# Kernel tuning notes

Hardware: AMD Instinct MI355X
Metric: run time of the kernel (lower is better)

Reference implementation:

```python
import jax, jax.numpy as jnp
import numpy as np

NUM_PERSISTENT = 16
ALIBI_ALPHA = 1.0
START_I = 0
DILATION = 1
LN_EPS = 1e-5


def setup_inputs() -> dict:
    key = jax.random.key(0)
    ks = jax.random.split(key, 16)
    B, S, C, H = 8, 1024, 512, 8
    D = C // H
    P = NUM_PERSISTENT
    Kk = 3
    x = jax.random.normal(ks[0], (B, S, C), dtype=jnp.float32)
    mask = jnp.ones((B, 1, S, S), dtype=jnp.int32)
    sc = 0.02
    Wq = jax.random.normal(ks[1], (D, D), jnp.float32) * sc
    Wk = jax.random.normal(ks[2], (D, D), jnp.float32) * sc
    Wv = jax.random.normal(ks[3], (D, D), jnp.float32) * sc
    pk = jax.random.normal(ks[4], (P, H, D), jnp.float32) * sc
    pv = jax.random.normal(ks[5], (P, H, D), jnp.float32) * sc
    th_pre = jax.random.normal(ks[6], (H, H), jnp.float32) * (1.0 / np.sqrt(H))
    th_post = jax.random.normal(ks[7], (H, H), jnp.float32) * (1.0 / np.sqrt(H))
    fc_w = jax.random.normal(ks[8], (C, C), jnp.float32) * sc
    fc_b = jnp.zeros((C,), jnp.float32)
    conv1_w = jax.random.normal(ks[9], (C, C, Kk), jnp.float32) * 0.01
    conv1_b = jnp.zeros((C,), jnp.float32)
    conv2_w = jax.random.normal(ks[10], (C, C, Kk), jnp.float32) * 0.01
    conv2_b = jnp.zeros((C,), jnp.float32)
    ln_g = jnp.ones((C,), jnp.float32)
    ln_b = jnp.zeros((C,), jnp.float32)
    return dict(x=x, mask=mask, Wq=Wq, Wk=Wk, Wv=Wv, pk=pk, pv=pv,
                th_pre=th_pre, th_post=th_post, fc_w=fc_w, fc_b=fc_b,
                conv1_w=conv1_w, conv1_b=conv1_b, conv2_w=conv2_w,
                conv2_b=conv2_b, ln_g=ln_g, ln_b=ln_b)


def _causal_conv(x_nct, w_oik, b_o, dilation):
    # padding (k-1)*d on both sides + chomp right == pad left only
    k = w_oik.shape[-1]
    p = (k - 1) * dilation
    y = jax.lax.conv_general_dilated(
        x_nct, w_oik, window_strides=(1,), padding=[(p, 0)],
        rhs_dilation=(dilation,), dimension_numbers=("NCH", "OIH", "NCH"))
    return y + b_o[None, :, None]


def reference(x, mask, Wq, Wk, Wv, pk, pv, th_pre, th_post, fc_w, fc_b,
              conv1_w, conv1_b, conv2_w, conv2_b, ln_g, ln_b):
    N, S, C = x.shape
    H = th_pre.shape[0]
    D = C // H
    P = pk.shape[0]

    # ---- MultiHeadAttention (eval: dropout = identity) ----
    xh = x.reshape(N, S, H, D)
    q = jnp.einsum("nshd,ed->nshe", xh, Wq)
    k = jnp.einsum("nshd,ed->nshe", xh, Wk)
    v = jnp.einsum("nshd,ed->nshe", xh, Wv)
    # persistent memory tokens appended along key/value length
    k = jnp.concatenate([k, jnp.broadcast_to(pk[None], (N, P, H, D))], axis=1)
    v = jnp.concatenate([v, jnp.broadcast_to(pv[None], (N, P, H, D))], axis=1)

    energy = jnp.einsum("nqhd,nkhd->nhqk", q, k)  # (N,H,S,S+P)

    # ALiBi bias (symmetric |q-k|), zero over persistent keys
    slopes = 2.0 ** (-(ALIBI_ALPHA * (jnp.arange(1, H + 1, dtype=jnp.float32) + START_I)))
    t = jnp.arange(S, dtype=jnp.float32)
    dist = jnp.abs(t[:, None] - t[None, :])  # (S,S)
    bias = -dist[None, None] * slopes[None, :, None, None]  # (1,H,S,S)
    bias = jnp.pad(bias, ((0, 0), (0, 0), (0, 0), (0, P)))
    energy = energy + bias

    # pre-softmax talking heads (1x1 conv over head axis)
    energy = jnp.einsum("hg,ngqk->nhqk", th_pre, energy)

    ext_mask = jnp.pad(mask, ((0, 0), (0, 0), (0, 0), (0, P)), constant_values=1)
    energy = jnp.where(ext_mask == 0, jnp.float32(-1e4), energy)

    attn = jax.nn.softmax(energy / jnp.sqrt(jnp.float32(C)), axis=-1)
    attn = jnp.einsum("hg,ngqk->nhqk", th_post, attn)

    att_out = jnp.einsum("nhql,nlhd->nqhd", attn, v).reshape(N, S, C)
    att_out = att_out @ fc_w.T + fc_b

    x = x + att_out  # residual (dropout1 identity in eval)

    # ---- TemporalBlock (causal dilated convs, no SE since heads>0) ----
    xc = jnp.transpose(x, (0, 2, 1))  # (N,C,S)
    h = jax.nn.relu(_causal_conv(xc, conv1_w, conv1_b, DILATION))
    h = jax.nn.relu(_causal_conv(h, conv2_w, conv2_b, DILATION))
    out = jax.nn.relu(h + xc)  # downsample is None (in==out)

    # mask out invalid frames
    conv_mask = mask[:, 0, :, 0][:, None, :]  # (N,1,S)
    out = jnp.where(conv_mask == 0, 0.0, out)

    y = jnp.transpose(out, (0, 2, 1))  # (N,S,C)
    mu = jnp.mean(y, axis=-1, keepdims=True)
    var = jnp.mean(jnp.square(y - mu), axis=-1, keepdims=True)
    y = (y - mu) * jax.lax.rsqrt(var + LN_EPS) * ln_g + ln_b
    return y
```

## Files before the change

kernel.cpp:

```cpp
#include <hip/hip_runtime.h>
#include <hip/hip_bf16.h>

#define BN 8
#define SS 1024
#define CC 512
#define HH 8
#define DD 64
#define PP 16
#define KT 1040
#define KTE 1088

typedef __hip_bfloat16 bf16;
typedef unsigned char uchar;
typedef unsigned short ushort;
typedef unsigned int uint;
typedef __attribute__((ext_vector_type(8))) short short8;
typedef __attribute__((ext_vector_type(4))) float f32x4;
typedef __attribute__((ext_vector_type(2))) float f32x2;

__device__ __forceinline__ short f2s(float v){ bf16 b = __float2bfloat16(v); return *(short*)&b; }
__device__ __forceinline__ float s2f(short s){ bf16 b; *(short*)&b = s; return __bfloat162float(b); }
__device__ __forceinline__ uchar f2q(float v){
    return (uchar)__builtin_amdgcn_cvt_pk_fp8_f32(v, v, 0, false);
}
__device__ __forceinline__ float rfl(float x){
    return __int_as_float(__builtin_amdgcn_readfirstlane(__float_as_int(x)));
}

#define MFMA16(a,b,c)  __builtin_amdgcn_mfma_f32_16x16x32_bf16(a,b,c,0,0,0)
#define MFMAF8(a,b,c)  __builtin_amdgcn_mfma_f32_16x16x32_fp8_fp8(a,b,c,0,0,0)

__global__ __launch_bounds__(256) void prep_kernel(
    const float* __restrict__ fc_w, const float* __restrict__ c1w,
    const float* __restrict__ c2w, const float* __restrict__ Wq,
    const float* __restrict__ Wk, const float* __restrict__ Wv,
    const float* __restrict__ th_post,
    const float* __restrict__ pk, const float* __restrict__ pv,
    short* __restrict__ Bfc, uchar* __restrict__ Bc1,
    uchar* __restrict__ Bc2, short* __restrict__ Bqkv,
    uchar* __restrict__ kf, uchar* __restrict__ vt)
{
    int i = blockIdx.x*256 + threadIdx.x;
    const int NFC = 512*512, NCV = 512*1536, NQ = 3*64*64, NP = BN*HH*PP*DD;
    if (i < NFC) {
        int c = i >> 9, r = i & 511;
        int g = r >> 6, d = r & 63;
        float s = 0.f;
        #pragma unroll
        for (int h = 0; h < 8; ++h)
            s += fc_w[(size_t)c*512 + h*64 + d] * th_post[h*8 + g];
        Bfc[i] = f2s(s);
        return;
    }
    i -= NFC;
    if (i < NCV) {
        int o = i/1536, r = i%1536, dk = r>>9, ci = r&511;
        Bc1[i] = f2q(c1w[(o*512+ci)*3+dk] * 16.f); return;
    }
    i -= NCV;
    if (i < NCV) {
        int o = i/1536, r = i%1536, dk = r>>9, ci = r&511;
        Bc2[i] = f2q(c2w[(o*512+ci)*3+dk] * 16.f); return;
    }
    i -= NCV;
    if (i < NQ) {
        int w = i >> 12, rest = i & 4095;
        const float* W = (w==0)?Wq:(w==1)?Wk:Wv;
        Bqkv[i] = f2s(W[((rest>>6)&63)*64 + (rest&63)]);
        return;
    }
    i -= NQ;
    if (i < NP) {
        int d = i & 63, p = (i >> 6) & 15, h = (i >> 10) & 7, n = i >> 13;
        size_t src = ((size_t)p*HH + h)*DD + d;
        kf[(((size_t)(n*HH+h))*KT + SS + p)*DD + d] = f2q(pk[src]);
        vt[(((size_t)(n*HH+h))*DD + d)*KT + SS + p] = f2q(pv[src]);
    }
}

__global__ __launch_bounds__(256) void qkv_mfma(
    const float* __restrict__ x, const short* __restrict__ Bqkv,
    uchar* __restrict__ qf, uchar* __restrict__ kf, uchar* __restrict__ vt)
{
    __shared__ short Xs[64*72];
    __shared__ short Ws[192*72];
    const int tid = threadIdx.x;
    const int lin = blockIdx.x;
    const int xcd = lin & 7, slot = lin >> 3;
    const int m0 = (xcd*16 + (slot & 15))*64;
    const int h = slot >> 4;
    const int wave = tid >> 6, lane = tid & 63;
    const int lr = lane & 15, lq = lane >> 4;

    for (int i = tid; i < 1024; i += 256) {
        int r = i >> 4, cg = (i & 15)*4;
        float4 v = *(const float4*)(x + (size_t)(m0+r)*CC + h*64 + cg);
        Xs[r*72+cg+0] = f2s(v.x); Xs[r*72+cg+1] = f2s(v.y);
        Xs[r*72+cg+2] = f2s(v.z); Xs[r*72+cg+3] = f2s(v.w);
    }
    for (int i = tid; i < 3072; i += 256) {
        int r = i >> 4, cg = (i & 15)*4;
        *(short4*)(Ws + r*72 + cg) = *(const short4*)(Bqkv + (size_t)r*64 + cg);
    }
    __syncthreads();

    f32x4 acc[12];
    #pragma unroll
    for (int nt = 0; nt < 12; ++nt) acc[nt] = {0.f,0.f,0.f,0.f};
    #pragma unroll
    for (int ks = 0; ks < 2; ++ks) {
        int ko = ks*32 + lq*8;
        short8 a = *(const short8*)(Xs + (wave*16 + lr)*72 + ko);
        #pragma unroll
        for (int nt = 0; nt < 12; ++nt) {
            short8 b = *(const short8*)(Ws + (nt*16 + lr)*72 + ko);
            acc[nt] = MFMA16(a, b, acc[nt]);
        }
    }
    #pragma unroll
    for (int nt = 0; nt < 12; ++nt) {
        int ep = nt*16 + lr;
        int w = ep >> 6, e = ep & 63;
        #pragma unroll
        for (int reg = 0; reg < 4; ++reg) {
            int m = m0 + wave*16 + lq*4 + reg;
            int n = m >> 10, s = m & 1023;
            float v = acc[nt][reg];
            if (w == 0)      qf[((size_t)(n*HH+h)*SS + s)*DD + e] = f2q(v);
            else if (w == 1) kf[((size_t)(n*HH+h)*KT + s)*DD + e] = f2q(v);
            else             vt[(((size_t)(n*HH+h))*DD + e)*KT + s] = f2q(v);
        }
    }
}

__device__ __forceinline__ void en_loadK(const uchar* __restrict__ kf,
    int nh, int kt, int tid, uint2* rk)
{
    #pragma unroll
    for (int j = 0; j < 2; ++j) {
        int i = tid + j*256;
        int r = i >> 3, c8 = (i & 7)*8;
        int kcol = kt*64 + r;
        uint2 v = {0u, 0u};
        if (kcol < KT)
            v = *(const uint2*)(kf + ((size_t)nh*KT + kcol)*DD + c8);
        rk[j] = v;
    }
}

__global__ __launch_bounds__(256) void energy_mfma8(
    const uchar* __restrict__ qf, const uchar* __restrict__ kf,
    uchar* __restrict__ E)
{
    __shared__ uchar Qs[64*72];
    __shared__ uchar Ks[64*72];
    const int tid = threadIdx.x;
    const int lin = blockIdx.x + 16*blockIdx.y;
    const int xcd = lin & 7, slot = lin >> 3;
    const int nh = xcd*8 + (slot & 7);
    const int mt = slot >> 3;
    const int wave = tid >> 6, lane = tid & 63;
    const int lr = lane & 15, lq = lane >> 4;
    const int n = nh >> 3, h = nh & 7;

    #pragma unroll
    for (int j = 0; j < 2; ++j) {
        int i = tid + j*256;
        int r = i >> 3, c8 = (i & 7)*8;
        *(uint2*)(Qs + r*72 + c8) =
            *(const uint2*)(qf + ((size_t)nh*SS + mt*64 + r)*DD + c8);
    }

    uint2 rk[2];
    en_loadK(kf, nh, 0, tid, rk);

    for (int kt = 0; kt < 17; ++kt) {
        if (kt) __syncthreads();
        #pragma unroll
        for (int j = 0; j < 2; ++j) {
            int i = tid + j*256;
            *(uint2*)(Ks + (i >> 3)*72 + (i & 7)*8) = rk[j];
        }
        __syncthreads();
        if (kt + 1 < 17) en_loadK(kf, nh, kt+1, tid, rk);

        f32x4 acc[4];
        #pragma unroll
        for (int nt = 0; nt < 4; ++nt) acc[nt] = {0.f,0.f,0.f,0.f};
        #pragma unroll
        for (int ks = 0; ks < 2; ++ks) {
            int ko = ks*32 + lq*8;
            long a = *(const long*)(Qs + (wave*16 + lr)*72 + ko);
            #pragma unroll
            for (int nt = 0; nt < 4; ++nt) {
                long b = *(const long*)(Ks + (nt*16 + lr)*72 + ko);
                acc[nt] = MFMAF8(a, b, acc[nt]);
            }
        }
        #pragma unroll
        for (int nt = 0; nt < 4; ++nt) {
            int kcol = kt*64 + nt*16 + lr;
            if (kcol >= KT) continue;
            #pragma unroll
            for (int reg = 0; reg < 4; ++reg) {
                int q = mt*64 + wave*16 + lq*4 + reg;
                E[(((size_t)(n*SS + q))*HH + h)*KTE + kcol] = f2q(acc[nt][reg]);
            }
        }
    }
}

__global__ __launch_bounds__(256, 2) void pv_fused(
    const uchar* __restrict__ E, const uchar* __restrict__ vt,
    const int* __restrict__ mask, const float* __restrict__ th_pre,
    short* __restrict__ AO)
{
    __shared__ uchar Ps[8*16*72];
    __shared__ float Sred[16][8];
    const int tid  = threadIdx.x;
    const int n    = blockIdx.x;
    const int ql0  = blockIdx.y * 16;
    const int wave = tid >> 6, lane = tid & 63;
    const int lr = lane & 15, lq = lane >> 4;
    const int q_l = lane >> 2, kc = lane & 3;
    const int q  = ql0 + q_l;
    const int hb = wave*2;

    const float sc = 0.044194173824159216f * 1.4426950408889634f;
    float tw[2][8], slmix[2], shf[2];
    {
        const float slv[8] = {0.5f,0.25f,0.125f,0.0625f,
                              0.03125f,0.015625f,0.0078125f,0.00390625f};
        const float maxd = (float)((q > SS-1-q) ? q : (SS-1-q));
        #pragma unroll
        for (int j = 0; j < 2; ++j) {
            float sm = 0.f;
            #pragma unroll
            for (int g = 0; g < 8; ++g) {
                float v = rfl(th_pre[(hb+j)*8+g] * sc);
                tw[j][g] = v;
                sm += v * slv[g];
            }
            slmix[j] = rfl(sm);
            shf[j] = fmaxf(0.f, -slmix[j] * maxd);
        }
    }

    const uchar* Eb  = E  + ((size_t)(n*SS + q))*HH*KTE;
    const uchar* Vh0 = vt + ((size_t)(n*HH) + hb + 0)*DD*KT;
    const uchar* Vh1 = vt + ((size_t)(n*HH) + hb + 1)*DD*KT;
    const int*  mrow = mask + (size_t)n*SS*SS + (size_t)q*SS;
    uchar* Ps0 = Ps + (hb+0)*1152;
    uchar* Ps1 = Ps + (hb+1)*1152;

    float sums[2] = {0.f, 0.f};
    f32x4 acc[2][4];
    #pragma unroll
    for (int i = 0; i < 2; ++i)
        #pragma unroll
        for (int j = 0; j < 4; ++j) acc[i][j] = {0.f,0.f,0.f,0.f};

    for (int kt = 0; kt < 17; ++kt) {
        const int kb = kt*64;
        long bva[2][4];
        #pragma unroll
        for (int ks = 0; ks < 2; ++ks)
            #pragma unroll
            for (int nt = 0; nt < 4; ++nt)
                bva[ks][nt] = *(const long*)(Vh0 + (size_t)(nt*16+lr)*KT + kb + ks*32 + lq*8);

        const bool body = (kt < 16);
        #pragma unroll
        for (int s = 0; s < 2; ++s) {
            const int k0 = kb + kc*16 + s*8;
            const bool valid = (k0 < KT);
            int4 rmA = {1,1,1,1}, rmB = {1,1,1,1};
            if (body) {
                rmA = *(const int4*)(mrow + k0);
                rmB = *(const int4*)(mrow + k0 + 4);
            }
            f32x4 tA[2], tB[2];
            if (body) {
                const float qv = (float)q, kf0 = (float)k0;
                f32x4 dA, dB;
                dA.x = fabsf(qv-kf0);      dA.y = fabsf(qv-kf0-1.f);
                dA.z = fabsf(qv-kf0-2.f);  dA.w = fabsf(qv-kf0-3.f);
                dB.x = fabsf(qv-kf0-4.f);  dB.y = fabsf(qv-kf0-5.f);
                dB.z = fabsf(qv-kf0-6.f);  dB.w = fabsf(qv-kf0-7.f);
                #pragma unroll
                for (int j = 0; j < 2; ++j) {
                    tA[j] = -dA*slmix[j] - shf[j];
                    tB[j] = -dB*slmix[j] - shf[j];
                }
            } else {
                #pragma unroll
                for (int j = 0; j < 2; ++j) {
                    tA[j] = {-shf[j],-shf[j],-shf[j],-shf[j]};
                    tB[j] = tA[j];
                }
            }
            #pragma unroll
            for (int g = 0; g < 8; ++g) {
                uint2 av = *(const uint2*)(Eb + (size_t)g*KTE + k0);
                f32x2 lo0 = __builtin_amdgcn_cvt_pk_f32_fp8((int)av.x, false);
                f32x2 hi0 = __builtin_amdgcn_cvt_pk_f32_fp8((int)av.x, true);
                f32x2 lo1 = __builtin_amdgcn_cvt_pk_f32_fp8((int)av.y, false);
                f32x2 hi1 = __builtin_amdgcn_cvt_pk_f32_fp8((int)av.y, true);
                f32x4 aA; aA.x=lo0.x; aA.y=lo0.y; aA.z=hi0.x; aA.w=hi0.y;
                f32x4 aB; aB.x=lo1.x; aB.y=lo1.y; aB.z=hi1.x; aB.w=hi1.y;
                #pragma unroll
                for (int j = 0; j < 2; ++j) {
                    tA[j] += aA * tw[j][g];
                    tB[j] += aB * tw[j][g];
                }
            }
            #pragma unroll
            for (int j = 0; j < 2; ++j) {
                f32x4 eA, eB;
                if (body) {
                    eA.x = (rmA.x==0)?0.f:exp2f(tA[j].x);
                    eA.y = (rmA.y==0)?0.f:exp2f(tA[j].y);
                    eA.z = (rmA.z==0)?0.f:exp2f(tA[j].z);
                    eA.w = (rmA.w==0)?0.f:exp2f(tA[j].w);
                    eB.x = (rmB.x==0)?0.f:exp2f(tB[j].x);
                    eB.y = (rmB.y==0)?0.f:exp2f(tB[j].y);
                    eB.z = (rmB.z==0)?0.f:exp2f(tB[j].z);
                    eB.w = (rmB.w==0)?0.f:exp2f(tB[j].w);
                } else if (valid) {
                    eA.x = exp2f(tA[j].x); eA.y = exp2f(tA[j].y);
                    eA.z = exp2f(tA[j].z); eA.w = exp2f(tA[j].w);
                    eB.x = exp2f(tB[j].x); eB.y = exp2f(tB[j].y);
                    eB.z = exp2f(tB[j].z); eB.w = exp2f(tB[j].w);
                } else {
                    eA = {0.f,0.f,0.f,0.f}; eB = {0.f,0.f,0.f,0.f};
                }
                sums[j] += (eA.x+eA.y)+(eA.z+eA.w) + (eB.x+eB.y)+(eB.z+eB.w);
                int p0 = __builtin_amdgcn_cvt_pk_fp8_f32(eA.x, eA.y, 0, false);
                p0 = __builtin_amdgcn_cvt_pk_fp8_f32(eA.z, eA.w, p0, true);
                int p1 = __builtin_amdgcn_cvt_pk_fp8_f32(eB.x, eB.y, 0, false);
                p1 = __builtin_amdgcn_cvt_pk_fp8_f32(eB.z, eB.w, p1, true);
                uint2 pw; pw.x = (uint)p0; pw.y = (uint)p1;
                uchar* dst = (j ? Ps1 : Ps0) + q_l*72 + kc*16 + s*8;
                *(uint2*)dst = pw;
            }
        }

        long bvb[2][4];
        #pragma unroll
        for (int ks = 0; ks < 2; ++ks)
            #pragma unroll
            for (int nt = 0; nt < 4; ++nt)
                bvb[ks][nt] = *(const long*)(Vh1 + (size_t)(nt*16+lr)*KT + kb + ks*32 + lq*8);

        #pragma unroll
        for (int ks = 0; ks < 2; ++ks) {
            int ko = ks*32 + lq*8;
            long av0 = *(const long*)(Ps0 + lr*72 + ko);
            #pragma unroll
            for (int nt = 0; nt < 4; ++nt)
                acc[0][nt] = MFMAF8(av0, bva[ks][nt], acc[0][nt]);
            long av1 = *(const long*)(Ps1 + lr*72 + ko);
            #pragma unroll
            for (int nt = 0; nt < 4; ++nt)
                acc[1][nt] = MFMAF8(av1, bvb[ks][nt], acc[1][nt]);
        }
    }

    #pragma unroll
    for (int j = 0; j < 2; ++j) {
        float s = sums[j];
        s += __shfl_xor(s, 1); s += __shfl_xor(s, 2);
        if (kc == 0) Sred[q_l][hb+j] = 1.0f / s;
    }

    #pragma unroll
    for (int h2 = 0; h2 < 2; ++h2) {
        int h = hb + h2;
        #pragma unroll
        for (int reg = 0; reg < 4; ++reg) {
            float inv = Sred[lq*4 + reg][h];
            int qg = ql0 + lq*4 + reg;
            #pragma unroll
            for (int nt = 0; nt < 4; ++nt) {
                int d = nt*16 + lr;
                AO[((size_t)(n*SS) + qg)*CC + h*64 + d] =
                    f2s(acc[h2][nt][reg] * inv);
            }
        }
    }
}

__device__ __forceinline__ void g_load4(const short* __restrict__ src,
    size_t rowstride, int row0, int col0, int tid, short4* r)
{
    #pragma unroll
    for (int j = 0; j < 4; ++j) {
        int i = tid + j*256;
        int rr = i >> 4, cg = (i & 15)*4;
        r[j] = *(const short4*)(src + (size_t)(row0 + rr)*rowstride + col0 + cg);
    }
}
__device__ __forceinline__ void lds_store4(short* __restrict__ dst,
    int tid, const short4* r)
{
    #pragma unroll
    for (int j = 0; j < 4; ++j) {
        int i = tid + j*256;
        *(short4*)(dst + (i >> 4)*72 + (i & 15)*4) = r[j];
    }
}

__global__ __launch_bounds__(256) void fc_mfma(
    const short* __restrict__ A, const short* __restrict__ Bt,
    const float* __restrict__ bias, const float* __restrict__ x,
    short* __restrict__ out, uchar* __restrict__ out8)
{
    __shared__ short As[64*72];
    __shared__ short Bs[64*72];
    const int tid = threadIdx.x;
    const int lin = blockIdx.x + 8*blockIdx.y;
    const int xcd = lin & 7, slot = lin >> 3;
    const int m0 = (xcd*16 + (slot & 15))*64;
    const int n0 = (slot >> 4)*64;
    const int wave = tid >> 6, lane = tid & 63;
    const int lr = lane & 15, lq = lane >> 4;

    short4 ra[4], rb[4];
    g_load4(A, CC, m0, 0, tid, ra);
    g_load4(Bt, CC, n0, 0, tid, rb);

    f32x4 acc[4];
    #pragma unroll
    for (int nt = 0; nt < 4; ++nt) acc[nt] = {0.f,0.f,0.f,0.f};

    for (int kt = 0; kt < CC; kt += 64) {
        if (kt) __syncthreads();
        lds_store4(As, tid, ra);
        lds_store4(Bs, tid, rb);
        __syncthreads();
        if (kt + 64 < CC) {
            g_load4(A, CC, m0, kt+64, tid, ra);
            g_load4(Bt, CC, n0, kt+64, tid, rb);
        }
        #pragma unroll
        for (int ks = 0; ks < 2; ++ks) {
            int ko = ks*32 + lq*8;
            short8 a = *(const short8*)(As + (wave*16 + lr)*72 + ko);
            #pragma unroll
            for (int nt = 0; nt < 4; ++nt) {
                short8 b = *(const short8*)(Bs + (nt*16 + lr)*72 + ko);
                acc[nt] = MFMA16(a, b, acc[nt]);
            }
        }
    }
    #pragma unroll
    for (int nt = 0; nt < 4; ++nt) {
        int nn = n0 + nt*16 + lr;
        #pragma unroll
        for (int reg = 0; reg < 4; ++reg) {
            int m = m0 + wave*16 + lq*4 + reg;
            float v = acc[nt][reg] + bias[nn] + x[(size_t)m*CC + nn];
            out[(size_t)m*CC + nn]  = f2s(v);
            out8[(size_t)m*CC + nn] = f2q(v);
        }
    }
}

__device__ __forceinline__ void conv_loadA8w(const uchar* __restrict__ A,
    int m0, int kt, int tid, uint2* ra)
{
    const int shift = (kt >> 9) - 2;
    const int ci0 = kt & 511;
    #pragma unroll
    for (int j = 0; j < 4; ++j) {
        int i = tid + j*256;
        int rr = i >> 4, c8 = (i & 15)*8;
        int m = m0 + rr;
        int s = m & (SS-1);
        uint2 v = {0u, 0u};
        if (s + shift >= 0)
            v = *(const uint2*)(A + (size_t)(m + shift)*CC + ci0 + c8);
        ra[j] = v;
    }
}
__device__ __forceinline__ void g_load8w(const uchar* __restrict__ src,
    size_t rowstride, int row0, int col0, int tid, uint2* r)
{
    #pragma unroll
    for (int j = 0; j < 4; ++j) {
        int i = tid + j*256;
        int rr = i >> 4, c8 = (i & 15)*8;
        r[j] = *(const uint2*)(src + (size_t)(row0 + rr)*rowstride + col0 + c8);
    }
}
__device__ __forceinline__ void lds_store8w(uchar* __restrict__ dst,
    int tid, const uint2* r)
{
    #pragma unroll
    for (int j = 0; j < 4; ++j) {
        int i = tid + j*256;
        *(uint2*)(dst + (i >> 4)*136 + (i & 15)*8) = r[j];
    }
}

__global__ __launch_bounds__(256) void conv_mfma8(
    const uchar* __restrict__ A, const uchar* __restrict__ Bt,
    const float* __restrict__ bias, uchar* __restrict__ out8,
    short* __restrict__ out16, int f8out)
{
    __shared__ uchar As[64*136];
    __shared__ uchar Bs[64*136];
    const int tid = threadIdx.x;
    const int lin = blockIdx.x + 8*blockIdx.y;
    const int xcd = lin & 7, slot = lin >> 3;
    const int m0 = (xcd*16 + (slot & 15))*64;
    const int n0 = (slot >> 4)*64;
    const int wave = tid >> 6, lane = tid & 63;
    const int lr = lane & 15, lq = lane >> 4;

    uint2 ra[4], rb[4];
    conv_loadA8w(A, m0, 0, tid, ra);
    g_load8w(Bt, 1536, n0, 0, tid, rb);

    f32x4 acc[4];
    #pragma unroll
    for (int nt = 0; nt < 4; ++nt) acc[nt] = {0.f,0.f,0.f,0.f};

    for (int kt = 0; kt < 1536; kt += 128) {
        if (kt) __syncthreads();
        lds_store8w(As, tid, ra);
        lds_store8w(Bs, tid, rb);
        __syncthreads();
        if (kt + 128 < 1536) {
            conv_loadA8w(A, m0, kt+128, tid, ra);
            g_load8w(Bt, 1536, n0, kt+128, tid, rb);
        }
        #pragma unroll
        for (int ks = 0; ks < 4; ++ks) {
            int ko = ks*32 + lq*8;
            long a = *(const long*)(As + (wave*16 + lr)*136 + ko);
            #pragma unroll
            for (int nt = 0; nt < 4; ++nt) {
                long b = *(const long*)(Bs + (nt*16 + lr)*136 + ko);
                acc[nt] = MFMAF8(a, b, acc[nt]);
            }
        }
    }
    #pragma unroll
    for (int nt = 0; nt < 4; ++nt) {
        int nn = n0 + nt*16 + lr;
        #pragma unroll
        for (int reg = 0; reg < 4; ++reg) {
            int m = m0 + wave*16 + lq*4 + reg;
            float v = fmaxf(acc[nt][reg]*0.0625f + bias[nn], 0.f);
            if (f8out) out8[(size_t)m*CC + nn]  = f2q(v);
            else       out16[(size_t)m*CC + nn] = f2s(v);
        }
    }
}

__global__ __launch_bounds__(256) void final_kernel(
    const short* __restrict__ c2, const short* __restrict__ xres,
    const int* __restrict__ mask, const float* __restrict__ g,
    const float* __restrict__ b, float* __restrict__ out)
{
    __shared__ float red[256];
    const int tid = threadIdx.x;
    const int m0 = blockIdx.x * 4;
    const int c0 = tid*2;
    const float2 gg = *(const float2*)(g + c0);
    const float2 bb = *(const float2*)(b + c0);

    for (int rr = 0; rr < 4; ++rr) {
        const int m = m0 + rr;
        const int n = m >> 10, s = m & 1023;
        const int mk = mask[(size_t)n*SS*SS + (size_t)s*SS];

        short2 ca = *(const short2*)(c2 + (size_t)m*CC + c0);
        short2 xa = *(const short2*)(xres + (size_t)m*CC + c0);
        float v0 = fmaxf(s2f(ca.x) + s2f(xa.x), 0.f);
        float v1 = fmaxf(s2f(ca.y) + s2f(xa.y), 0.f);
        if (mk == 0) { v0 = 0.f; v1 = 0.f; }

        red[tid] = v0 + v1;
        __syncthreads();
        for (int off = 128; off > 0; off >>= 1) {
            if (tid < off) red[tid] += red[tid + off];
            __syncthreads();
        }
        float mu = red[0] * (1.0f/512.0f);
        __syncthreads();
        float d0 = v0 - mu, d1 = v1 - mu;
        red[tid] = d0*d0 + d1*d1;
        __syncthreads();
        for (int off = 128; off > 0; off >>= 1) {
            if (tid < off) red[tid] += red[tid + off];
            __syncthreads();
        }
        float rstd = rsqrtf(red[0] * (1.0f/512.0f) + 1e-5f);
        float2 o;
        o.x = d0*rstd*gg.x + bb.x;
        o.y = d1*rstd*gg.y + bb.y;
        *(float2*)(out + (size_t)m*CC + c0) = o;
        __syncthreads();
    }
}

extern "C" void kernel_launch(void* const* d_in, const int* in_sizes, int n_in,
                              void* d_out, int out_size, void* d_ws, size_t ws_size,
                              hipStream_t stream)
{
    const float* x      = (const float*)d_in[0];
    const int*   mask   = (const int*)  d_in[1];
    const float* Wq     = (const float*)d_in[2];
    const float* Wk     = (const float*)d_in[3];
    const float* Wv     = (const float*)d_in[4];
    const float* pk     = (const float*)d_in[5];
    const float* pv     = (const float*)d_in[6];
    const float* th_pre = (const float*)d_in[7];
    const float* th_post= (const float*)d_in[8];
    const float* fc_w   = (const float*)d_in[9];
    const float* fc_b   = (const float*)d_in[10];
    const float* c1w    = (const float*)d_in[11];
    const float* c1b    = (const float*)d_in[12];
    const float* c2w    = (const float*)d_in[13];
    const float* c2b    = (const float*)d_in[14];
    const float* lng    = (const float*)d_in[15];
    const float* lnb    = (const float*)d_in[16];
    float* out = (float*)d_out;
    (void)in_sizes; (void)n_in; (void)out_size; (void)ws_size;

    char* ws = (char*)d_ws;
    const size_t SZ_Q  = (size_t)BN*HH*SS*DD;
    const size_t SZ_K  = (size_t)BN*HH*KT*DD;
    const size_t SZ_VT = (size_t)BN*HH*DD*KT;
    const size_t SZ_E  = (size_t)BN*SS*HH*KTE;
    const size_t SZ_A  = (size_t)BN*SS*CC*2;
    const size_t SZ_A8 = (size_t)BN*SS*CC;

    uchar* qf  = (uchar*)(ws);
    uchar* kf  = (uchar*)(ws + SZ_Q);
    uchar* vt  = (uchar*)(ws + SZ_Q + SZ_K);
    uchar* E   = (uchar*)(ws + SZ_Q + SZ_K + SZ_VT);
    short* AO  = (short*)(ws + SZ_Q + SZ_K + SZ_VT + SZ_E);
    char*  wend = ws + SZ_Q + SZ_K + SZ_VT + SZ_E + SZ_A;
    short* Bfc = (short*)(wend);
    uchar* Bc1 = (uchar*)(wend + 512*512*2);
    uchar* Bc2 = (uchar*)(wend + 512*512*2 + 512*1536);
    short* Bqkv= (short*)(wend + 512*512*2 + 2*512*1536);
    uchar* xres8 = (uchar*)(wend + 512*512*2 + 2*512*1536 + 3*64*64*2);
    short* c2buf = (short*)(wend + 512*512*2 + 2*512*1536 + 3*64*64*2 + SZ_A8);
    short* xres = (short*)(ws);
    uchar* h18  = (uchar*)E;

    {
        int total = 512*512 + 2*512*1536 + 3*64*64 + BN*HH*PP*DD;
        prep_kernel<<<(total + 255)/256, 256, 0, stream>>>(
            fc_w, c1w, c2w, Wq, Wk, Wv, th_post, pk, pv,
            Bfc, Bc1, Bc2, Bqkv, kf, vt);
    }
    qkv_mfma<<<BN*SS/64*HH, 256, 0, stream>>>(x, Bqkv, qf, kf, vt);

    energy_mfma8<<<dim3(16, 64), 256, 0, stream>>>(qf, kf, E);
    pv_fused<<<dim3(8, 64), 256, 0, stream>>>(E, vt, mask, th_pre, AO);

    fc_mfma<<<dim3(8, 128), 256, 0, stream>>>(AO, Bfc, fc_b, x, xres, xres8);
    conv_mfma8<<<dim3(8, 128), 256, 0, stream>>>(xres8, Bc1, c1b, h18, (short*)nullptr, 1);
    conv_mfma8<<<dim3(8, 128), 256, 0, stream>>>(h18, Bc2, c2b, (uchar*)nullptr, c2buf, 0);
    final_kernel<<<BN*SS/4, 256, 0, stream>>>(c2buf, xres, mask, lng, lnb, out);
}
```

Measured before the change: 299.9 us.

## Assign one head per wave in pv_fused with 512-thread blocks and batched loads

The fused softmax-PV kernel now launches 512 threads so each of the 8 waves handles one head instead of two, halving per-wave serial work and register state. The per-tile E and mask reads are hoisted into wide 16-byte loads issued before the compute loop rather than 8-byte loads inside it. The aim is more waves in flight to hide memory latency and fewer load instructions. In exchange, every wave redundantly loads the same mask and recomputes the distance terms, and launch bounds now target four 512-thread blocks per CU, which caps registers per thread.

```diff
diff --git a/kernel.cpp b/kernel.cpp
--- a/kernel.cpp
+++ b/kernel.cpp
@@ -210,7 +210,7 @@
     }
 }
 
-__global__ __launch_bounds__(256, 2) void pv_fused(
+__global__ __launch_bounds__(512, 4) void pv_fused(
     const uchar* __restrict__ E, const uchar* __restrict__ vt,
     const int* __restrict__ mask, const float* __restrict__ th_pre,
     short* __restrict__ AO)
@@ -220,66 +220,67 @@
     const int tid  = threadIdx.x;
     const int n    = blockIdx.x;
     const int ql0  = blockIdx.y * 16;
-    const int wave = tid >> 6, lane = tid & 63;
+    const int h    = tid >> 6;
+    const int lane = tid & 63;
     const int lr = lane & 15, lq = lane >> 4;
     const int q_l = lane >> 2, kc = lane & 3;
     const int q  = ql0 + q_l;
-    const int hb = wave*2;
+    const int kcol0 = kc*16;
 
     const float sc = 0.044194173824159216f * 1.4426950408889634f;
-    float tw[2][8], slmix[2], shf[2];
+    float tw[8], slmix, shf;
     {
         const float slv[8] = {0.5f,0.25f,0.125f,0.0625f,
                               0.03125f,0.015625f,0.0078125f,0.00390625f};
         const float maxd = (float)((q > SS-1-q) ? q : (SS-1-q));
-        #pragma unroll
-        for (int j = 0; j < 2; ++j) {
-            float sm = 0.f;
-            #pragma unroll
-            for (int g = 0; g < 8; ++g) {
-                float v = rfl(th_pre[(hb+j)*8+g] * sc);
-                tw[j][g] = v;
-                sm += v * slv[g];
-            }
-            slmix[j] = rfl(sm);
-            shf[j] = fmaxf(0.f, -slmix[j] * maxd);
-        }
+        float sm = 0.f;
+        #pragma unroll
+        for (int g = 0; g < 8; ++g) {
+            float v = rfl(th_pre[h*8+g] * sc);
+            tw[g] = v;
+            sm += v * slv[g];
+        }
+        slmix = rfl(sm);
+        shf = fmaxf(0.f, -slmix * maxd);
     }
 
     const uchar* Eb  = E  + ((size_t)(n*SS + q))*HH*KTE;
-    const uchar* Vh0 = vt + ((size_t)(n*HH) + hb + 0)*DD*KT;
-    const uchar* Vh1 = vt + ((size_t)(n*HH) + hb + 1)*DD*KT;
+    const uchar* Vh  = vt + ((size_t)(n*HH) + h)*DD*KT;
     const int*  mrow = mask + (size_t)n*SS*SS + (size_t)q*SS;
-    uchar* Ps0 = Ps + (hb+0)*1152;
-    uchar* Ps1 = Ps + (hb+1)*1152;
-
-    float sums[2] = {0.f, 0.f};
-    f32x4 acc[2][4];
-    #pragma unroll
-    for (int i = 0; i < 2; ++i)
-        #pragma unroll
-        for (int j = 0; j < 4; ++j) acc[i][j] = {0.f,0.f,0.f,0.f};
+    uchar* Psh = Ps + h*1152;
+
+    float sums = 0.f;
+    f32x4 acc[4];
+    #pragma unroll
+    for (int j = 0; j < 4; ++j) acc[j] = {0.f,0.f,0.f,0.f};
 
     for (int kt = 0; kt < 17; ++kt) {
         const int kb = kt*64;
+        const bool body = (kt < 16);
+
         long bva[2][4];
         #pragma unroll
         for (int ks = 0; ks < 2; ++ks)
             #pragma unroll
             for (int nt = 0; nt < 4; ++nt)
-                bva[ks][nt] = *(const long*)(Vh0 + (size_t)(nt*16+lr)*KT + kb + ks*32 + lq*8);
-
-        const bool body = (kt < 16);
+                bva[ks][nt] = *(const long*)(Vh + (size_t)(nt*16+lr)*KT + kb + ks*32 + lq*8);
+
+        uint4 rE[8];
+        #pragma unroll
+        for (int g = 0; g < 8; ++g)
+            rE[g] = *(const uint4*)(Eb + (size_t)g*KTE + kb + kcol0);
+        int4 rm[4];
+        if (body) {
+            #pragma unroll
+            for (int j = 0; j < 4; ++j)
+                rm[j] = *(const int4*)(mrow + kb + kcol0 + j*4);
+        }
+
         #pragma unroll
         for (int s = 0; s < 2; ++s) {
-            const int k0 = kb + kc*16 + s*8;
+            const int k0 = kb + kcol0 + s*8;
             const bool valid = (k0 < KT);
-            int4 rmA = {1,1,1,1}, rmB = {1,1,1,1};
-            if (body) {
-                rmA = *(const int4*)(mrow + k0);
-                rmB = *(const int4*)(mrow + k0 + 4);
-            }
-            f32x4 tA[2], tB[2];
+            f32x4 tA, tB;
             if (body) {
                 const float qv = (float)q, kf0 = (float)k0;
                 f32x4 dA, dB;
@@ -287,105 +288,77 @@
                 dA.z = fabsf(qv-kf0-2.f);  dA.w = fabsf(qv-kf0-3.f);
                 dB.x = fabsf(qv-kf0-4.f);  dB.y = fabsf(qv-kf0-5.f);
                 dB.z = fabsf(qv-kf0-6.f);  dB.w = fabsf(qv-kf0-7.f);
-                #pragma unroll
-                for (int j = 0; j < 2; ++j) {
-                    tA[j] = -dA*slmix[j] - shf[j];
-                    tB[j] = -dB*slmix[j] - shf[j];
-                }
+                tA = -dA*slmix - shf;
+                tB = -dB*slmix - shf;
             } else {
-                #pragma unroll
-                for (int j = 0; j < 2; ++j) {
-                    tA[j] = {-shf[j],-shf[j],-shf[j],-shf[j]};
-                    tB[j] = tA[j];
-                }
+                tA = {-shf,-shf,-shf,-shf};
+                tB = tA;
             }
             #pragma unroll
             for (int g = 0; g < 8; ++g) {
-                uint2 av = *(const uint2*)(Eb + (size_t)g*KTE + k0);
-                f32x2 lo0 = __builtin_amdgcn_cvt_pk_f32_fp8((int)av.x, false);
-                f32x2 hi0 = __builtin_amdgcn_cvt_pk_f32_fp8((int)av.x, true);
-                f32x2 lo1 = __builtin_amdgcn_cvt_pk_f32_fp8((int)av.y, false);
-                f32x2 hi1 = __builtin_amdgcn_cvt_pk_f32_fp8((int)av.y, true);
+                const uint w0 = (s == 0) ? rE[g].x : rE[g].z;
+                const uint w1 = (s == 0) ? rE[g].y : rE[g].w;
+                f32x2 lo0 = __builtin_amdgcn_cvt_pk_f32_fp8((int)w0, false);
+                f32x2 hi0 = __builtin_amdgcn_cvt_pk_f32_fp8((int)w0, true);
+                f32x2 lo1 = __builtin_amdgcn_cvt_pk_f32_fp8((int)w1, false);
+                f32x2 hi1 = __builtin_amdgcn_cvt_pk_f32_fp8((int)w1, true);
                 f32x4 aA; aA.x=lo0.x; aA.y=lo0.y; aA.z=hi0.x; aA.w=hi0.y;
                 f32x4 aB; aB.x=lo1.x; aB.y=lo1.y; aB.z=hi1.x; aB.w=hi1.y;
-                #pragma unroll
-                for (int j = 0; j < 2; ++j) {
-                    tA[j] += aA * tw[j][g];
-                    tB[j] += aB * tw[j][g];
-                }
+                tA += aA * tw[g];
+                tB += aB * tw[g];
             }
-            #pragma unroll
-            for (int j = 0; j < 2; ++j) {
-                f32x4 eA, eB;
-                if (body) {
-                    eA.x = (rmA.x==0)?0.f:exp2f(tA[j].x);
-                    eA.y = (rmA.y==0)?0.f:exp2f(tA[j].y);
-                    eA.z = (rmA.z==0)?0.f:exp2f(tA[j].z);
-                    eA.w = (rmA.w==0)?0.f:exp2f(tA[j].w);
-                    eB.x = (rmB.x==0)?0.f:exp2f(tB[j].x);
-                    eB.y = (rmB.y==0)?0.f:exp2f(tB[j].y);
-                    eB.z = (rmB.z==0)?0.f:exp2f(tB[j].z);
-                    eB.w = (rmB.w==0)?0.f:exp2f(tB[j].w);
-                } else if (valid) {
-                    eA.x = exp2f(tA[j].x); eA.y = exp2f(tA[j].y);
-                    eA.z = exp2f(tA[j].z); eA.w = exp2f(tA[j].w);
-                    eB.x = exp2f(tB[j].x); eB.y = exp2f(tB[j].y);
-                    eB.z = exp2f(tB[j].z); eB.w = exp2f(tB[j].w);
-                } else {
-                    eA = {0.f,0.f,0.f,0.f}; eB = {0.f,0.f,0.f,0.f};
-                }
-                sums[j] += (eA.x+eA.y)+(eA.z+eA.w) + (eB.x+eB.y)+(eB.z+eB.w);
-                int p0 = __builtin_amdgcn_cvt_pk_fp8_f32(eA.x, eA.y, 0, false);
-                p0 = __builtin_amdgcn_cvt_pk_fp8_f32(eA.z, eA.w, p0, true);
-                int p1 = __builtin_amdgcn_cvt_pk_fp8_f32(eB.x, eB.y, 0, false);
-                p1 = __builtin_amdgcn_cvt_pk_fp8_f32(eB.z, eB.w, p1, true);
-                uint2 pw; pw.x = (uint)p0; pw.y = (uint)p1;
-                uchar* dst = (j ? Ps1 : Ps0) + q_l*72 + kc*16 + s*8;
-                *(uint2*)dst = pw;
+            f32x4 eA, eB;
+            if (body) {
+                const int4 rmA = rm[2*s], rmB = rm[2*s+1];
+                eA.x = (rmA.x==0)?0.f:exp2f(tA.x);
+                eA.y = (rmA.y==0)?0.f:exp2f(tA.y);
+                eA.z = (rmA.z==0)?0.f:exp2f(tA.z);
+                eA.w = (rmA.w==0)?0.f:exp2f(tA.w);
+                eB.x = (rmB.x==0)?0.f:exp2f(tB.x);
+                eB.y = (rmB.y==0)?0.f:exp2f(tB.y);
+                eB.z = (rmB.z==0)?0.f:exp2f(tB.z);
+                eB.w = (rmB.w==0)?0.f:exp2f(tB.w);
+            } else if (valid) {
+                eA.x = exp2f(tA.x); eA.y = exp2f(tA.y);
+                eA.z = exp2f(tA.z); eA.w = exp2f(tA.w);
+                eB.x = exp2f(tB.x); eB.y = exp2f(tB.y);
+                eB.z = exp2f(tB.z); eB.w = exp2f(tB.w);
+            } else {
+                eA = {0.f,0.f,0.f,0.f}; eB = {0.f,0.f,0.f,0.f};
             }
-        }
-
-        long bvb[2][4];
-        #pragma unroll
-        for (int ks = 0; ks < 2; ++ks)
-            #pragma unroll
-            for (int nt = 0; nt < 4; ++nt)
-                bvb[ks][nt] = *(const long*)(Vh1 + (size_t)(nt*16+lr)*KT + kb + ks*32 + lq*8);
+            sums += (eA.x+eA.y)+(eA.z+eA.w) + (eB.x+eB.y)+(eB.z+eB.w);
+            int p0 = __builtin_amdgcn_cvt_pk_fp8_f32(eA.x, eA.y, 0, false);
+            p0 = __builtin_amdgcn_cvt_pk_fp8_f32(eA.z, eA.w, p0, true);
+            int p1 = __builtin_amdgcn_cvt_pk_fp8_f32(eB.x, eB.y, 0, false);
+            p1 = __builtin_amdgcn_cvt_pk_fp8_f32(eB.z, eB.w, p1, true);
+            uint2 pw; pw.x = (uint)p0; pw.y = (uint)p1;
+            *(uint2*)(Psh + q_l*72 + kcol0 + s*8) = pw;
+        }
 
         #pragma unroll
         for (int ks = 0; ks < 2; ++ks) {
             int ko = ks*32 + lq*8;
-            long av0 = *(const long*)(Ps0 + lr*72 + ko);
+            long av = *(const long*)(Psh + lr*72 + ko);
             #pragma unroll
             for (int nt = 0; nt < 4; ++nt)
-                acc[0][nt] = MFMAF8(av0, bva[ks][nt], acc[0][nt]);
-            long av1 = *(const long*)(Ps1 + lr*72 + ko);
-            #pragma unroll
-            for (int nt = 0; nt < 4; ++nt)
-                acc[1][nt] = MFMAF8(av1, bvb[ks][nt], acc[1][nt]);
-        }
-    }
-
-    #pragma unroll
-    for (int j = 0; j < 2; ++j) {
-        float s = sums[j];
+                acc[nt] = MFMAF8(av, bva[ks][nt], acc[nt]);
+        }
+    }
+
+    {
+        float s = sums;
         s += __shfl_xor(s, 1); s += __shfl_xor(s, 2);
-        if (kc == 0) Sred[q_l][hb+j] = 1.0f / s;
-    }
-
-    #pragma unroll
-    for (int h2 = 0; h2 < 2; ++h2) {
-        int h = hb + h2;
-        #pragma unroll
-        for (int reg = 0; reg < 4; ++reg) {
-            float inv = Sred[lq*4 + reg][h];
-            int qg = ql0 + lq*4 + reg;
-            #pragma unroll
-            for (int nt = 0; nt < 4; ++nt) {
-                int d = nt*16 + lr;
-                AO[((size_t)(n*SS) + qg)*CC + h*64 + d] =
-                    f2s(acc[h2][nt][reg] * inv);
-            }
+        if (kc == 0) Sred[q_l][h] = 1.0f / s;
+    }
+
+    #pragma unroll
+    for (int reg = 0; reg < 4; ++reg) {
+        float inv = Sred[lq*4 + reg][h];
+        int qg = ql0 + lq*4 + reg;
+        #pragma unroll
+        for (int nt = 0; nt < 4; ++nt) {
+            int d = nt*16 + lr;
+            AO[((size_t)(n*SS) + qg)*CC + h*64 + d] = f2s(acc[nt][reg] * inv);
         }
     }
 }
@@ -662,7 +635,7 @@
     qkv_mfma<<<BN*SS/64*HH, 256, 0, stream>>>(x, Bqkv, qf, kf, vt);
 
     energy_mfma8<<<dim3(16, 64), 256, 0, stream>>>(qf, kf, E);
-    pv_fused<<<dim3(8, 64), 256, 0, stream>>>(E, vt, mask, th_pre, AO);
+    pv_fused<<<dim3(8, 64), 512, 0, stream>>>(E, vt, mask, th_pre, AO);
 
     fc_mfma<<<dim3(8, 128), 256, 0, stream>>>(AO, Bfc, fc_b, x, xres, xres8);
     conv_mfma8<<<dim3(8, 128), 256, 0, stream>>>(xres8, Bc1, c1b, h18, (short*)nullptr, 1);
```

New measurement: 331.6 us. 10.6% more time.
